# Kernel tuning notes

Hardware: AMD Instinct MI355X
Metric: run time of the kernel (lower is better)

The kernel has to match this reference:

```python
import jax, jax.numpy as jnp
import numpy as np

EPS = 1e-12
B, CNT = 4096, 2048

def setup_inputs() -> dict:
    key = jax.random.key(0)
    k1, k2, k3 = jax.random.split(key, 3)
    timestampns_set = jax.random.uniform(k1, (B, CNT), dtype=jnp.float32)
    gyro_set = jax.random.normal(k2, (B, CNT, 3), dtype=jnp.float32)
    start_quat = jax.random.normal(k3, (B, 4), dtype=jnp.float32)
    # conv1/conv2 reduce to 3x3 linear maps on the xyz axis; initialized to identity, bias 0
    W1 = jnp.eye(3, dtype=jnp.float32)
    b1 = jnp.zeros((3,), dtype=jnp.float32)
    a1 = jnp.float32(0.25)  # PReLU default, single shared parameter
    W2 = jnp.eye(3, dtype=jnp.float32)
    b2 = jnp.zeros((3,), dtype=jnp.float32)
    a2 = jnp.float32(0.25)
    return {"timestampns_set": timestampns_set, "gyro_set": gyro_set,
            "start_quat": start_quat, "W1": W1, "b1": b1, "a1": a1,
            "W2": W2, "b2": b2, "a2": a2}

def _prelu(x, a):
    return jnp.where(x >= 0, x, a * x)

def _qmul(a, b):
    aw, ax, ay, az = a[:, 0], a[:, 1], a[:, 2], a[:, 3]
    bw, bx, by, bz = b[:, 0], b[:, 1], b[:, 2], b[:, 3]
    ow = aw * bw - ax * bx - ay * by - az * bz
    ox = aw * bx + ax * bw + ay * bz - az * by
    oy = aw * by - ax * bz + ay * bw + az * bx
    oz = aw * bz + ax * by - ay * bx + az * bw
    return jnp.stack((ow, ox, oy, oz), axis=-1)

def reference(timestampns_set, gyro_set, start_quat, W1, b1, a1, W2, b2, a2):
    # calibrate_gyro: two identity-init 3x3 'convs' + PReLU, residual add
    h = _prelu(jnp.einsum('btc,oc->bto', gyro_set, W1) + b1, a1)
    g = _prelu(jnp.einsum('btc,oc->bto', h, W2) + b2, a2) + gyro_set  # [B,CNT,3]
    dt = timestampns_set[:, 1:] - timestampns_set[:, :-1]             # [B,CNT-1]
    gm = 0.5 * (g[:, :-1, :] + g[:, 1:, :])                            # midpoint gyro
    dtheta_half = gm * dt[:, :, None] * 0.5                           # [B,CNT-1,3]

    def step(q, d):
        dq = jnp.concatenate([jnp.ones((d.shape[0], 1), d.dtype), d], axis=1)
        q = _qmul(q, dq)
        n = jnp.sqrt(jnp.sum(q * q, axis=1, keepdims=True))
        q = q / jnp.maximum(n, EPS)  # F.normalize semantics
        return q, None

    q, _ = jax.lax.scan(step, start_quat, jnp.swapaxes(dtheta_half, 0, 1))
    return q
```

## Files before the change

### kernel.cpp

```cpp
#include <hip/hip_runtime.h>

#define CNT   2048
#define TPB   256
#define CHUNK 8
#define NWAVE (TPB / 64)

struct Q { float w, x, y, z; };

__device__ __forceinline__ Q qmul(const Q a, const Q b) {
    Q o;
    o.w = fmaf(a.w, b.w, fmaf(-a.x, b.x, fmaf(-a.y, b.y, -a.z * b.z)));
    o.x = fmaf(a.w, b.x, fmaf( a.x, b.w, fmaf( a.y, b.z, -a.z * b.y)));
    o.y = fmaf(a.w, b.y, fmaf(-a.x, b.z, fmaf( a.y, b.w,  a.z * b.x)));
    o.z = fmaf(a.w, b.z, fmaf( a.x, b.y, fmaf(-a.y, b.x,  a.z * b.w)));
    return o;
}

__device__ __forceinline__ Q qmul1(const Q a, const float bx, const float by, const float bz) {
    Q o;
    o.w = fmaf(-a.x, bx, fmaf(-a.y, by, fmaf(-a.z, bz, a.w)));
    o.x = fmaf( a.w, bx, fmaf( a.y, bz, fmaf(-a.z, by, a.x)));
    o.y = fmaf( a.w, by, fmaf(-a.x, bz, fmaf( a.z, bx, a.y)));
    o.z = fmaf( a.w, bz, fmaf( a.x, by, fmaf(-a.y, bx, a.z)));
    return o;
}

__device__ __forceinline__ float prelu(const float x, const float a, const float one_m_a) {
    return fmaf(one_m_a, fmaxf(x, 0.0f), a * x);
}

__global__ __launch_bounds__(TPB) void quat_scan_kernel(
    const float* __restrict__ ts,
    const float* __restrict__ gyro,
    const float* __restrict__ sq,
    const float* __restrict__ W1, const float* __restrict__ b1, const float* __restrict__ a1p,
    const float* __restrict__ W2, const float* __restrict__ b2, const float* __restrict__ a2p,
    float* __restrict__ out)
{
    __shared__ Q s_q[NWAVE];

    const int  b    = blockIdx.x;
    const int  tid  = threadIdx.x;
    const int  t0   = tid * CHUNK;
    const bool last = (tid == TPB - 1);

    float g[28];
    {
        const float4* gp = (const float4*)(gyro + (size_t)b * (CNT * 3) + 3 * t0);
        #pragma unroll
        for (int k = 0; k < 6; ++k) ((float4*)g)[k] = gp[k];
        const float4* g6 = gp + (last ? 5 : 6);
        ((float4*)g)[6] = *g6;
    }

    float rt[9];
    {
        const float4* tp = (const float4*)(ts + (size_t)b * CNT + t0);
        ((float4*)rt)[0] = tp[0];
        ((float4*)rt)[1] = tp[1];
        const int i8 = last ? (t0 + 7) : (t0 + 8);
        rt[8] = ts[(size_t)b * CNT + i8];
    }

    float w1[9], w2[9], bb1[3], bb2[3];
    #pragma unroll
    for (int i = 0; i < 9; ++i) { w1[i] = W1[i]; w2[i] = W2[i]; }
    #pragma unroll
    for (int i = 0; i < 3; ++i) { bb1[i] = b1[i]; bb2[i] = b2[i]; }
    const float a1 = a1p[0], a2 = a2p[0];
    const float oma1 = 1.0f - a1, oma2 = 1.0f - a2;

    auto gf = [&](const int j, float& gx, float& gy, float& gz) {
        const float vx = g[3 * j + 0];
        const float vy = g[3 * j + 1];
        const float vz = g[3 * j + 2];
        float h0 = fmaf(w1[0], vx, fmaf(w1[1], vy, fmaf(w1[2], vz, bb1[0])));
        float h1 = fmaf(w1[3], vx, fmaf(w1[4], vy, fmaf(w1[5], vz, bb1[1])));
        float h2 = fmaf(w1[6], vx, fmaf(w1[7], vy, fmaf(w1[8], vz, bb1[2])));
        h0 = prelu(h0, a1, oma1);
        h1 = prelu(h1, a1, oma1);
        h2 = prelu(h2, a1, oma1);
        float u0 = fmaf(w2[0], h0, fmaf(w2[1], h1, fmaf(w2[2], h2, bb2[0])));
        float u1 = fmaf(w2[3], h0, fmaf(w2[4], h1, fmaf(w2[5], h2, bb2[1])));
        float u2 = fmaf(w2[6], h0, fmaf(w2[7], h1, fmaf(w2[8], h2, bb2[2])));
        gx = prelu(u0, a2, oma2) + vx;
        gy = prelu(u1, a2, oma2) + vy;
        gz = prelu(u2, a2, oma2) + vz;
    };

    Q q = {1.0f, 0.0f, 0.0f, 0.0f};
    float g0x, g0y, g0z;
    gf(0, g0x, g0y, g0z);
    #pragma unroll
    for (int j = 0; j < CHUNK; ++j) {
        float g1x, g1y, g1z;
        gf(j + 1, g1x, g1y, g1z);
        const float s = 0.25f * (rt[j + 1] - rt[j]);
        q = qmul1(q, (g0x + g1x) * s, (g0y + g1y) * s, (g0z + g1z) * s);
        g0x = g1x; g0y = g1y; g0z = g1z;
    }

    {
        const float n2  = fmaf(q.w, q.w, fmaf(q.x, q.x, fmaf(q.y, q.y, q.z * q.z)));
        const float inv = 1.0f / sqrtf(n2);
        q.w *= inv; q.x *= inv; q.y *= inv; q.z *= inv;
    }

    #pragma unroll
    for (int sft = 1; sft < 64; sft <<= 1) {
        Q o;
        o.w = __shfl_down(q.w, sft);
        o.x = __shfl_down(q.x, sft);
        o.y = __shfl_down(q.y, sft);
        o.z = __shfl_down(q.z, sft);
        q = qmul(q, o);
    }

    const int lane = tid & 63;
    const int wid  = tid >> 6;
    if (lane == 0) s_q[wid] = q;
    __syncthreads();

    if (tid == 0) {
        Q acc = s_q[0];
        #pragma unroll
        for (int w = 1; w < NWAVE; ++w) acc = qmul(acc, s_q[w]);

        const float4 s0 = ((const float4*)(sq + (size_t)b * 4))[0];
        const Q q0 = {s0.x, s0.y, s0.z, s0.w};
        Q qf = qmul(q0, acc);
        const float n   = sqrtf(fmaf(qf.w, qf.w, fmaf(qf.x, qf.x, fmaf(qf.y, qf.y, qf.z * qf.z))));
        const float inv = 1.0f / fmaxf(n, 1e-12f);
        float4 o;
        o.x = qf.w * inv; o.y = qf.x * inv; o.z = qf.y * inv; o.w = qf.z * inv;
        ((float4*)(out + (size_t)b * 4))[0] = o;
    }
}

extern "C" void kernel_launch(void* const* d_in, const int* in_sizes, int n_in,
                              void* d_out, int out_size, void* d_ws, size_t ws_size,
                              hipStream_t stream) {
    const float* ts   = (const float*)d_in[0];
    const float* gyro = (const float*)d_in[1];
    const float* sq   = (const float*)d_in[2];
    const float* W1   = (const float*)d_in[3];
    const float* b1   = (const float*)d_in[4];
    const float* a1   = (const float*)d_in[5];
    const float* W2   = (const float*)d_in[6];
    const float* b2   = (const float*)d_in[7];
    const float* a2   = (const float*)d_in[8];
    float* out = (float*)d_out;

    const int B = in_sizes[0] / CNT;

    quat_scan_kernel<<<B, TPB, 0, stream>>>(ts, gyro, sq, W1, b1, a1, W2, b2, a2, out);
}
```

Measured before the change: 184.8 us.

## Assign one wavefront per batch row with 32 steps per lane

Each batch row is now handled by a single 64-lane wavefront instead of a 256-thread block, with four rows per block. Each lane processes 32 timesteps in four macro-chunks of eight. Every chunk loads its gyro and timestamp window as float4 reads, with index clamping at the row end. This removes the shared-memory cross-wave combine and the block barrier, and lets lane 0 finalize each row directly. In exchange there are four times fewer threads, a longer serial chain per lane and more register pressure, which may hurt latency hiding.

```diff
diff --git a/kernel.cpp b/kernel.cpp
--- a/kernel.cpp
+++ b/kernel.cpp
@@ -2,8 +2,9 @@
 
 #define CNT   2048
 #define TPB   256
-#define CHUNK 8
-#define NWAVE (TPB / 64)
+#define RPB   4
+#define NMAC  4
+#define MAC   8
 
 struct Q { float w, x, y, z; };
 
@@ -35,32 +36,13 @@
     const float* __restrict__ sq,
     const float* __restrict__ W1, const float* __restrict__ b1, const float* __restrict__ a1p,
     const float* __restrict__ W2, const float* __restrict__ b2, const float* __restrict__ a2p,
-    float* __restrict__ out)
+    float* __restrict__ out,
+    const int B)
 {
-    __shared__ Q s_q[NWAVE];
-
-    const int  b    = blockIdx.x;
-    const int  tid  = threadIdx.x;
-    const int  t0   = tid * CHUNK;
-    const bool last = (tid == TPB - 1);
-
-    float g[28];
-    {
-        const float4* gp = (const float4*)(gyro + (size_t)b * (CNT * 3) + 3 * t0);
-        #pragma unroll
-        for (int k = 0; k < 6; ++k) ((float4*)g)[k] = gp[k];
-        const float4* g6 = gp + (last ? 5 : 6);
-        ((float4*)g)[6] = *g6;
-    }
-
-    float rt[9];
-    {
-        const float4* tp = (const float4*)(ts + (size_t)b * CNT + t0);
-        ((float4*)rt)[0] = tp[0];
-        ((float4*)rt)[1] = tp[1];
-        const int i8 = last ? (t0 + 7) : (t0 + 8);
-        rt[8] = ts[(size_t)b * CNT + i8];
-    }
+    const int lane = threadIdx.x & 63;
+    const int wid  = threadIdx.x >> 6;
+    const int row  = blockIdx.x * RPB + wid;
+    if (row >= B) return;
 
     float w1[9], w2[9], bb1[3], bb2[3];
     #pragma unroll
@@ -70,10 +52,8 @@
     const float a1 = a1p[0], a2 = a2p[0];
     const float oma1 = 1.0f - a1, oma2 = 1.0f - a2;
 
-    auto gf = [&](const int j, float& gx, float& gy, float& gz) {
-        const float vx = g[3 * j + 0];
-        const float vy = g[3 * j + 1];
-        const float vz = g[3 * j + 2];
+    auto gfv = [&](const float vx, const float vy, const float vz,
+                   float& gx, float& gy, float& gz) {
         float h0 = fmaf(w1[0], vx, fmaf(w1[1], vy, fmaf(w1[2], vz, bb1[0])));
         float h1 = fmaf(w1[3], vx, fmaf(w1[4], vy, fmaf(w1[5], vz, bb1[1])));
         float h2 = fmaf(w1[6], vx, fmaf(w1[7], vy, fmaf(w1[8], vz, bb1[2])));
@@ -88,16 +68,55 @@
         gz = prelu(u2, a2, oma2) + vz;
     };
 
+    const float4* gp = (const float4*)(gyro + (size_t)row * (CNT * 3));
+    const float4* tp = (const float4*)(ts   + (size_t)row * CNT);
+    const int gbase = 24 * lane;
+    const int tbase = 8  * lane;
+
     Q q = {1.0f, 0.0f, 0.0f, 0.0f};
     float g0x, g0y, g0z;
-    gf(0, g0x, g0y, g0z);
+
     #pragma unroll
-    for (int j = 0; j < CHUNK; ++j) {
-        float g1x, g1y, g1z;
-        gf(j + 1, g1x, g1y, g1z);
-        const float s = 0.25f * (rt[j + 1] - rt[j]);
-        q = qmul1(q, (g0x + g1x) * s, (g0y + g1y) * s, (g0z + g1z) * s);
-        g0x = g1x; g0y = g1y; g0z = g1z;
+    for (int m = 0; m < NMAC; ++m) {
+        float4 Gv[7];
+        #pragma unroll
+        for (int k = 0; k < 7; ++k) {
+            int gi = gbase + 6 * m + k;
+            gi = gi > (CNT * 3 / 4 - 1) ? (CNT * 3 / 4 - 1) : gi;
+            Gv[k] = gp[gi];
+        }
+        float4 Tv[3];
+        #pragma unroll
+        for (int k = 0; k < 3; ++k) {
+            int ti = tbase + 2 * m + k;
+            ti = ti > (CNT / 4 - 1) ? (CNT / 4 - 1) : ti;
+            Tv[k] = tp[ti];
+        }
+
+        float gg[28];
+        #pragma unroll
+        for (int k = 0; k < 7; ++k) {
+            gg[4*k+0] = Gv[k].x; gg[4*k+1] = Gv[k].y;
+            gg[4*k+2] = Gv[k].z; gg[4*k+3] = Gv[k].w;
+        }
+        float rtw[12];
+        #pragma unroll
+        for (int k = 0; k < 3; ++k) {
+            rtw[4*k+0] = Tv[k].x; rtw[4*k+1] = Tv[k].y;
+            rtw[4*k+2] = Tv[k].z; rtw[4*k+3] = Tv[k].w;
+        }
+        if (m == NMAC - 1) rtw[8] = (lane == 63) ? rtw[7] : rtw[8];
+
+        if (m == 0) gfv(gg[0], gg[1], gg[2], g0x, g0y, g0z);
+
+        #pragma unroll
+        for (int u = 0; u < MAC; ++u) {
+            float g1x, g1y, g1z;
+            gfv(gg[3*u+3], gg[3*u+4], gg[3*u+5], g1x, g1y, g1z);
+            const float s = 0.25f * (rtw[u + 1] - rtw[u]);
+            q = qmul1(q, (g0x + g1x) * s, (g0y + g1y) * s, (g0z + g1z) * s);
+            g0x = g1x; g0y = g1y; g0z = g1z;
+        }
     }
 
     {
@@ -116,24 +135,15 @@
         q = qmul(q, o);
     }
 
-    const int lane = tid & 63;
-    const int wid  = tid >> 6;
-    if (lane == 0) s_q[wid] = q;
-    __syncthreads();
-
-    if (tid == 0) {
-        Q acc = s_q[0];
-        #pragma unroll
-        for (int w = 1; w < NWAVE; ++w) acc = qmul(acc, s_q[w]);
-
-        const float4 s0 = ((const float4*)(sq + (size_t)b * 4))[0];
+    if (lane == 0) {
+        const float4 s0 = ((const float4*)(sq + (size_t)row * 4))[0];
         const Q q0 = {s0.x, s0.y, s0.z, s0.w};
-        Q qf = qmul(q0, acc);
+        Q qf = qmul(q0, q);
         const float n   = sqrtf(fmaf(qf.w, qf.w, fmaf(qf.x, qf.x, fmaf(qf.y, qf.y, qf.z * qf.z))));
         const float inv = 1.0f / fmaxf(n, 1e-12f);
         float4 o;
         o.x = qf.w * inv; o.y = qf.x * inv; o.z = qf.y * inv; o.w = qf.z * inv;
-        ((float4*)(out + (size_t)b * 4))[0] = o;
+        ((float4*)(out + (size_t)row * 4))[0] = o;
     }
 }
 
@@ -152,6 +162,7 @@
     float* out = (float*)d_out;
 
     const int B = in_sizes[0] / CNT;
+    const int grid = (B + RPB - 1) / RPB;
 
-    quat_scan_kernel<<<B, TPB, 0, stream>>>(ts, gyro, sq, W1, b1, a1, W2, b2, a2, out);
+    quat_scan_kernel<<<grid, TPB, 0, stream>>>(ts, gyro, sq, W1, b1, a1, W2, b2, a2, out, B);
 }
```

After: 202.5 us. 1.1x slower.

## Split each row scan across two blocks and combine halves in a second kernel

Applied to the files above, without the earlier changes.

Each batch row is now processed by two blocks, each handling 1024 timesteps with 4 steps per thread instead of 8. Partial quaternions are normalized and written to workspace, and a small combine kernel multiplies the halves with the start quaternion. The intent is to cut per-thread register pressure (launch bounds now request 8 blocks) and raise parallelism and memory-level concurrency on a bandwidth-bound kernel. The cost is an extra kernel launch, a workspace round trip, and more shuffle-reduction work relative to the number of timesteps.

```diff
diff --git a/kernel.cpp b/kernel.cpp
--- a/kernel.cpp
+++ b/kernel.cpp
@@ -2,7 +2,7 @@
 
 #define CNT   2048
 #define TPB   256
-#define CHUNK 8
+#define CH    4
 #define NWAVE (TPB / 64)
 
 struct Q { float w, x, y, z; };
@@ -29,38 +29,31 @@
     return fmaf(one_m_a, fmaxf(x, 0.0f), a * x);
 }
 
-__global__ __launch_bounds__(TPB) void quat_scan_kernel(
+__global__ __launch_bounds__(TPB, 8) void half_scan_kernel(
     const float* __restrict__ ts,
     const float* __restrict__ gyro,
-    const float* __restrict__ sq,
     const float* __restrict__ W1, const float* __restrict__ b1, const float* __restrict__ a1p,
     const float* __restrict__ W2, const float* __restrict__ b2, const float* __restrict__ a2p,
-    float* __restrict__ out)
+    float* __restrict__ ws)
 {
     __shared__ Q s_q[NWAVE];
 
-    const int  b    = blockIdx.x;
-    const int  tid  = threadIdx.x;
-    const int  t0   = tid * CHUNK;
-    const bool last = (tid == TPB - 1);
+    const int tid  = threadIdx.x;
+    const int bid  = blockIdx.x;
+    const int row  = bid >> 1;
+    const int S0   = ((bid & 1) << 10) + tid * CH;
+    const bool last = (S0 + CH >= CNT);
 
-    float g[28];
-    {
-        const float4* gp = (const float4*)(gyro + (size_t)b * (CNT * 3) + 3 * t0);
-        #pragma unroll
-        for (int k = 0; k < 6; ++k) ((float4*)g)[k] = gp[k];
-        const float4* g6 = gp + (last ? 5 : 6);
-        ((float4*)g)[6] = *g6;
-    }
-
-    float rt[9];
-    {
-        const float4* tp = (const float4*)(ts + (size_t)b * CNT + t0);
-        ((float4*)rt)[0] = tp[0];
-        ((float4*)rt)[1] = tp[1];
-        const int i8 = last ? (t0 + 7) : (t0 + 8);
-        rt[8] = ts[(size_t)b * CNT + i8];
-    }
+    const float4* gp4 = (const float4*)(gyro + (size_t)row * (CNT * 3));
+    const float4* tp4 = (const float4*)(ts   + (size_t)row * CNT);
+    const int q0 = (3 * S0) >> 2;
+    const float4 Ga = gp4[q0];
+    const float4 Gb = gp4[q0 + 1];
+    const float4 Gc = gp4[q0 + 2];
+    const float4 Gd = gp4[last ? (q0 + 2) : (q0 + 3)];
+    const int t0 = S0 >> 2;
+    const float4 Tv = tp4[t0];
+    const float4 Tw = tp4[last ? t0 : (t0 + 1)];
 
     float w1[9], w2[9], bb1[3], bb2[3];
     #pragma unroll
@@ -70,10 +63,8 @@
     const float a1 = a1p[0], a2 = a2p[0];
     const float oma1 = 1.0f - a1, oma2 = 1.0f - a2;
 
-    auto gf = [&](const int j, float& gx, float& gy, float& gz) {
-        const float vx = g[3 * j + 0];
-        const float vy = g[3 * j + 1];
-        const float vz = g[3 * j + 2];
+    auto gfv = [&](const float vx, const float vy, const float vz,
+                   float& gx, float& gy, float& gz) {
         float h0 = fmaf(w1[0], vx, fmaf(w1[1], vy, fmaf(w1[2], vz, bb1[0])));
         float h1 = fmaf(w1[3], vx, fmaf(w1[4], vy, fmaf(w1[5], vz, bb1[1])));
         float h2 = fmaf(w1[6], vx, fmaf(w1[7], vy, fmaf(w1[8], vz, bb1[2])));
@@ -88,17 +79,31 @@
         gz = prelu(u2, a2, oma2) + vz;
     };
 
+    const float gw0  = Ga.x, gw1  = Ga.y, gw2  = Ga.z, gw3  = Ga.w;
+    const float gw4  = Gb.x, gw5  = Gb.y, gw6  = Gb.z, gw7  = Gb.w;
+    const float gw8  = Gc.x, gw9  = Gc.y, gw10 = Gc.z, gw11 = Gc.w;
+    const float gw12 = Gd.x, gw13 = Gd.y, gw14 = Gd.z;
+    const float rt0 = Tv.x, rt1 = Tv.y, rt2 = Tv.z, rt3 = Tv.w;
+    const float rt4 = last ? Tv.w : Tw.x;
+
     Q q = {1.0f, 0.0f, 0.0f, 0.0f};
-    float g0x, g0y, g0z;
-    gf(0, g0x, g0y, g0z);
-    #pragma unroll
-    for (int j = 0; j < CHUNK; ++j) {
-        float g1x, g1y, g1z;
-        gf(j + 1, g1x, g1y, g1z);
-        const float s = 0.25f * (rt[j + 1] - rt[j]);
-        q = qmul1(q, (g0x + g1x) * s, (g0y + g1y) * s, (g0z + g1z) * s);
-        g0x = g1x; g0y = g1y; g0z = g1z;
-    }
+    float ax, ay, az, bx, by, bz;
+    gfv(gw0, gw1, gw2, ax, ay, az);
+    gfv(gw3, gw4, gw5, bx, by, bz);
+    { const float s = 0.25f * (rt1 - rt0);
+      q = qmul1(q, (ax + bx) * s, (ay + by) * s, (az + bz) * s); }
+    ax = bx; ay = by; az = bz;
+    gfv(gw6, gw7, gw8, bx, by, bz);
+    { const float s = 0.25f * (rt2 - rt1);
+      q = qmul1(q, (ax + bx) * s, (ay + by) * s, (az + bz) * s); }
+    ax = bx; ay = by; az = bz;
+    gfv(gw9, gw10, gw11, bx, by, bz);
+    { const float s = 0.25f * (rt3 - rt2);
+      q = qmul1(q, (ax + bx) * s, (ay + by) * s, (az + bz) * s); }
+    ax = bx; ay = by; az = bz;
+    gfv(gw12, gw13, gw14, bx, by, bz);
+    { const float s = 0.25f * (rt4 - rt3);
+      q = qmul1(q, (ax + bx) * s, (ay + by) * s, (az + bz) * s); }
 
     {
         const float n2  = fmaf(q.w, q.w, fmaf(q.x, q.x, fmaf(q.y, q.y, q.z * q.z)));
@@ -125,16 +130,35 @@
         Q acc = s_q[0];
         #pragma unroll
         for (int w = 1; w < NWAVE; ++w) acc = qmul(acc, s_q[w]);
+        const float n2  = fmaf(acc.w, acc.w, fmaf(acc.x, acc.x, fmaf(acc.y, acc.y, acc.z * acc.z)));
+        const float inv = 1.0f / sqrtf(n2);
+        float4 o;
+        o.x = acc.w * inv; o.y = acc.x * inv; o.z = acc.y * inv; o.w = acc.z * inv;
+        ((float4*)(ws + (size_t)bid * 4))[0] = o;
+    }
+}
 
-        const float4 s0 = ((const float4*)(sq + (size_t)b * 4))[0];
-        const Q q0 = {s0.x, s0.y, s0.z, s0.w};
-        Q qf = qmul(q0, acc);
-        const float n   = sqrtf(fmaf(qf.w, qf.w, fmaf(qf.x, qf.x, fmaf(qf.y, qf.y, qf.z * qf.z))));
-        const float inv = 1.0f / fmaxf(n, 1e-12f);
-        float4 o;
-        o.x = qf.w * inv; o.y = qf.x * inv; o.z = qf.y * inv; o.w = qf.z * inv;
-        ((float4*)(out + (size_t)b * 4))[0] = o;
-    }
+__global__ __launch_bounds__(TPB) void combine_kernel(
+    const float* __restrict__ ws,
+    const float* __restrict__ sq,
+    float* __restrict__ out,
+    const int B)
+{
+    const int i = blockIdx.x * TPB + threadIdx.x;
+    if (i >= B) return;
+    const float4 h0 = ((const float4*)(ws + (size_t)(2 * i)     * 4))[0];
+    const float4 h1 = ((const float4*)(ws + (size_t)(2 * i + 1) * 4))[0];
+    const Q a = {h0.x, h0.y, h0.z, h0.w};
+    const Q b = {h1.x, h1.y, h1.z, h1.w};
+    const Q full = qmul(a, b);
+    const float4 s0 = ((const float4*)(sq + (size_t)i * 4))[0];
+    const Q q0 = {s0.x, s0.y, s0.z, s0.w};
+    Q qf = qmul(q0, full);
+    const float n   = sqrtf(fmaf(qf.w, qf.w, fmaf(qf.x, qf.x, fmaf(qf.y, qf.y, qf.z * qf.z))));
+    const float inv = 1.0f / fmaxf(n, 1e-12f);
+    float4 o;
+    o.x = qf.w * inv; o.y = qf.x * inv; o.z = qf.y * inv; o.w = qf.z * inv;
+    ((float4*)(out + (size_t)i * 4))[0] = o;
 }
 
 extern "C" void kernel_launch(void* const* d_in, const int* in_sizes, int n_in,
@@ -150,8 +174,10 @@
     const float* b2   = (const float*)d_in[7];
     const float* a2   = (const float*)d_in[8];
     float* out = (float*)d_out;
+    float* ws  = (float*)d_ws;
 
     const int B = in_sizes[0] / CNT;
 
-    quat_scan_kernel<<<B, TPB, 0, stream>>>(ts, gyro, sq, W1, b1, a1, W2, b2, a2, out);
+    half_scan_kernel<<<2 * B, TPB, 0, stream>>>(ts, gyro, W1, b1, a1, W2, b2, a2, ws);
+    combine_kernel<<<(B + TPB - 1) / TPB, TPB, 0, stream>>>(ws, sq, out, B);
 }
```

After: 183.4 us. No clear change (-0.8%).
